# Performance work log

Hardware: AMD Instinct MI355X
Metric: run time of the kernel (lower is better)

## Reference

```python
import math
import jax, jax.numpy as jnp
import numpy as np

_EPS = 1e-8

def _nan_to_num(x):
    return jnp.where(jnp.isfinite(x), x, jnp.zeros((), x.dtype))

def _norm(x, axis=-1, keepdims=False):
    return jnp.sqrt(jnp.sum(x * x, axis=axis, keepdims=keepdims) + _EPS)

def _normalize(x, axis=-1):
    return _nan_to_num(x / _norm(x, axis=axis, keepdims=True))

def _dihedrals(X, eps=1e-7):
    # X: [B, N, A, 3]; use first 3 backbone atoms, flatten to [B, 3N, 3]
    B, N = X.shape[0], X.shape[1]
    Xf = X[:, :, :3].reshape(B, 3 * N, 3)
    dX = Xf[:, 1:] - Xf[:, :-1]
    U = _normalize(dX)
    u_2, u_1, u_0 = U[:, :-2], U[:, 1:-1], U[:, 2:]
    n_2 = _normalize(jnp.cross(u_2, u_1))
    n_1 = _normalize(jnp.cross(u_1, u_0))
    cosD = jnp.clip(jnp.sum(n_2 * n_1, -1), -1 + eps, 1 - eps)
    D = jnp.sign(jnp.sum(u_2 * n_1, -1)) * jnp.arccos(cosD)
    D = jnp.pad(D, ((0, 0), (1, 2)))
    D = D.reshape(B, N, 3)
    return jnp.concatenate([jnp.cos(D), jnp.sin(D)], axis=-1)  # [B, N, 6]

def _orientations(X):
    # X: [B, N, 3] (CA coords)
    fwd = _normalize(X[:, 1:] - X[:, :-1])
    bwd = _normalize(X[:, :-1] - X[:, 1:])
    fwd = jnp.pad(fwd, ((0, 0), (0, 1), (0, 0)))
    bwd = jnp.pad(bwd, ((0, 0), (1, 0), (0, 0)))
    return jnp.concatenate([fwd[:, :, None], bwd[:, :, None]], axis=-2)  # [B, N, 2, 3]

def _sidechains(X):
    n, origin, c = X[:, :, 0], X[:, :, 1], X[:, :, 2]
    c = _normalize(c - origin)
    n = _normalize(n - origin)
    bisector = _normalize(c + n)
    perp = _normalize(jnp.cross(c, n))
    return -bisector * math.sqrt(1.0 / 3.0) - perp * math.sqrt(2.0 / 3.0)  # [B, N, 3]

def _dist(X, coord_mask, res_idx, padding_mask, top_k, order=3):
    # X: [B, N, 3] CA coords
    B, N = X.shape[0], X.shape[1]
    cm2 = coord_mask[:, None, :] & coord_mask[:, :, None]        # [B, N, N]
    rm = ~padding_mask
    rm2 = rm[:, None, :] & rm[:, :, None]
    dX = X[:, None, :, :] - X[:, :, None, :]                     # [B, N, N, 3]
    D = cm2 * _norm(dX)                                          # masked pairwise dists
    cov = (jnp.abs(res_idx[..., None] - res_idx[..., None, :]) <= order).astype(D.dtype)
    D_cov = D * (1.0 - cov)
    seq = jnp.arange(N)
    Dseq = jnp.abs(seq[None, :] - seq[:, None]).astype(D.dtype)[None]  # [1, N, N]
    D_adjust = _nan_to_num(D_cov) + (~cm2) * (1e8 + Dseq * 1e6) + (~rm2) * 1e10
    k = min(int(top_k), N)
    # smallest-k via top_k on negated distances
    _, E_idx = jax.lax.top_k(-D_adjust, k)                       # [B, N, k]
    D_neighbors = jnp.take_along_axis(D, E_idx, axis=-1)
    coord_mask_neighbors = D_neighbors < 5e7
    residue_mask_neighbors = D_neighbors < 5e9
    return D_neighbors, E_idx, coord_mask_neighbors, residue_mask_neighbors


def setup_inputs() -> dict:
    key = jax.random.key(0)
    k1, k2 = jax.random.split(key)
    B, N = 8, 2048
    coords = jax.random.normal(k1, (B, N, 3, 3), dtype=jnp.float32) * 10.0
    coord_mask = jax.random.bernoulli(k2, 0.9, (B, N))
    res_idx = jnp.broadcast_to(jnp.arange(N, dtype=jnp.int32), (B, N))
    padding_mask = jnp.zeros((B, N), dtype=bool)
    return {"coords": coords, "coord_mask": coord_mask, "res_idx": res_idx,
            "padding_mask": padding_mask, "top_k": 30}


def reference(coords, coord_mask, res_idx, padding_mask, top_k):
    node_scalar = jnp.concatenate(
        [_dihedrals(coords), coord_mask.astype(jnp.float32)[..., None]], axis=-1)  # [B, N, 7]
    X_ca = coords[:, :, 1]
    orient = _orientations(X_ca)            # [B, N, 2, 3]
    side = _sidechains(coords)              # [B, N, 3]
    node_vector = jnp.concatenate([orient, side[:, :, None]], axis=-2)  # [B, N, 3, 3]
    D_neighbors, E_idx, cm_nb, rm_nb = _dist(X_ca, coord_mask, res_idx, padding_mask, top_k)
    return node_scalar, node_vector, D_neighbors, E_idx, cm_nb, rm_nb
```

## Files before the change

### kernel.cpp

```cpp
#include <hip/hip_runtime.h>

#define BB 8
#define NN 2048
#define KK 30
#define UNKV  0xFFFFFFFEu
#define EMPV  0xFFFFFFFFu
#define SENTJ 0xFFFFFFFFu
typedef unsigned long long ull;

__device__ __forceinline__ float norm3_eps_exact(float dx, float dy, float dz) {
    float s = __fadd_rn(__fadd_rn(__fmul_rn(dx, dx), __fmul_rn(dy, dy)), __fmul_rn(dz, dz));
    return __fsqrt_rn(__fadd_rn(s, 1e-8f));
}

__device__ __forceinline__ void normalize3f(float x, float y, float z, float* o) {
    float s = x * x + y * y + z * z + 1e-8f;
    float inv = __builtin_amdgcn_rsqf(s);
    o[0] = x * inv; o[1] = y * inv; o[2] = z * inv;
}

template <int CTRL>
__device__ __forceinline__ unsigned dppmin(unsigned v) {
    unsigned t = (unsigned)__builtin_amdgcn_update_dpp((int)v, (int)v, CTRL, 0xF, 0xF, false);
    return (t < v) ? t : v;
}
__device__ __forceinline__ unsigned wave_min_last(unsigned v) {
    v = dppmin<0xB1>(v);
    v = dppmin<0x4E>(v);
    v = dppmin<0x141>(v);
    v = dppmin<0x140>(v);
    v = dppmin<0x142>(v);
    v = dppmin<0x143>(v);
    return v;
}

__device__ __forceinline__ unsigned key_bits(const float4* __restrict__ Pb, int i, unsigned j,
                                             float xi, float yi, float zi, bool cmi_on) {
    int dd = i - (int)j;
    unsigned dj = (dd < 0) ? (unsigned)(-dd) : (unsigned)dd;
    float penB = __fadd_rn(1e8f, __fmul_rn((float)dj, 1e6f));
    float adj;
    if (cmi_on) {
        float4 p = Pb[j];
        bool cmj = ((int)__float_as_uint(p.w)) < 0;
        float nrm = norm3_eps_exact(p.x - xi, p.y - yi, p.z - zi);
        adj = cmj ? ((dj <= 3u) ? 0.0f : nrm) : penB;
    } else {
        adj = penB;
    }
    return __float_as_uint(adj);
}

__global__ __launch_bounds__(64) void prep_kernel(const float* __restrict__ coords,
                                                  const int* __restrict__ cmask,
                                                  float* __restrict__ out_scalar,
                                                  float* __restrict__ out_vec,
                                                  float4* __restrict__ P) {
    __shared__ float sm[66 * 9];
    int b  = blockIdx.x >> 5;
    int n0 = (blockIdx.x & 31) << 6;
    int tid = threadIdx.x;
    const float* gbase = coords + (size_t)b * NN * 9;
    int lof = (n0 - 1) * 9;
    for (int idx = tid; idx < 66 * 9; idx += 64) {
        int gidx = lof + idx;
        sm[idx] = ((unsigned)gidx < (unsigned)(NN * 9)) ? gbase[gidx] : 0.0f;
    }
    __syncthreads();

    const float* lbase = sm - lof;
    int n  = n0 + tid;
    int bn = b * NN + n;

    float cosv[3], sinv[3];
    #pragma unroll
    for (int t = 0; t < 3; ++t) {
        int m = 3 * n + t;
        if (m < 1 || m > 3 * NN - 3) { cosv[t] = 1.0f; sinv[t] = 0.0f; continue; }
        const float* p0 = lbase + (m - 1) * 3;
        const float* p1 = lbase + (m    ) * 3;
        const float* p2 = lbase + (m + 1) * 3;
        const float* p3 = lbase + (m + 2) * 3;
        float u2[3], u1[3], u0[3];
        normalize3f(p1[0]-p0[0], p1[1]-p0[1], p1[2]-p0[2], u2);
        normalize3f(p2[0]-p1[0], p2[1]-p1[1], p2[2]-p1[2], u1);
        normalize3f(p3[0]-p2[0], p3[1]-p2[1], p3[2]-p2[2], u0);
        float c21[3] = { u2[1]*u1[2]-u2[2]*u1[1], u2[2]*u1[0]-u2[0]*u1[2], u2[0]*u1[1]-u2[1]*u1[0] };
        float c10[3] = { u1[1]*u0[2]-u1[2]*u0[1], u1[2]*u0[0]-u1[0]*u0[2], u1[0]*u0[1]-u1[1]*u0[0] };
        float n2[3], n1v[3];
        normalize3f(c21[0], c21[1], c21[2], n2);
        normalize3f(c10[0], c10[1], c10[2], n1v);
        float cd = n2[0]*n1v[0] + n2[1]*n1v[1] + n2[2]*n1v[2];
        cd = fminf(fmaxf(cd, -1.0f + 1e-7f), 1.0f - 1e-7f);
        float sg = u2[0]*n1v[0] + u2[1]*n1v[1] + u2[2]*n1v[2];
        float sgn = (sg > 0.0f) ? 1.0f : ((sg < 0.0f) ? -1.0f : 0.0f);
        cosv[t] = (sgn == 0.0f) ? 1.0f : cd;
        sinv[t] = sgn * sqrtf(fmaxf(0.0f, 1.0f - cd * cd));
    }
    int cm = cmask[bn];
    float* os = out_scalar + (size_t)bn * 7;
    os[0] = cosv[0]; os[1] = cosv[1]; os[2] = cosv[2];
    os[3] = sinv[0]; os[4] = sinv[1]; os[5] = sinv[2];
    os[6] = cm ? 1.0f : 0.0f;

    const float* ca = lbase + (n * 3 + 1) * 3;
    float cx = ca[0], cy = ca[1], cz = ca[2];
    P[(size_t)b * NN + n] = make_float4(cx, cy, cz, __uint_as_float(cm ? 0x80000000u : 0u));

    float fwd[3] = {0.f, 0.f, 0.f}, bwd[3] = {0.f, 0.f, 0.f};
    if (n < NN - 1) {
        const float* cn = lbase + ((n + 1) * 3 + 1) * 3;
        normalize3f(cn[0]-cx, cn[1]-cy, cn[2]-cz, fwd);
    }
    if (n > 0) {
        const float* cp = lbase + ((n - 1) * 3 + 1) * 3;
        normalize3f(cp[0]-cx, cp[1]-cy, cp[2]-cz, bwd);
    }
    const float* pn = lbase + (n * 3 + 0) * 3;
    const float* pc = lbase + (n * 3 + 2) * 3;
    float cv[3], nv[3];
    normalize3f(pc[0]-cx, pc[1]-cy, pc[2]-cz, cv);
    normalize3f(pn[0]-cx, pn[1]-cy, pn[2]-cz, nv);
    float bis[3];
    normalize3f(cv[0]+nv[0], cv[1]+nv[1], cv[2]+nv[2], bis);
    float cr[3] = { cv[1]*nv[2]-cv[2]*nv[1], cv[2]*nv[0]-cv[0]*nv[2], cv[0]*nv[1]-cv[1]*nv[0] };
    float perp[3];
    normalize3f(cr[0], cr[1], cr[2], perp);
    const float s13 = 0.57735026918962576f;
    const float s23 = 0.81649658092772603f;
    float* ov = out_vec + (size_t)bn * 9;
    ov[0] = fwd[0]; ov[1] = fwd[1]; ov[2] = fwd[2];
    ov[3] = bwd[0]; ov[4] = bwd[1]; ov[5] = bwd[2];
    ov[6] = -bis[0]*s13 - perp[0]*s23;
    ov[7] = -bis[1]*s13 - perp[1]*s23;
    ov[8] = -bis[2]*s13 - perp[2]*s23;
}

__global__ __launch_bounds__(256, 8) void knn_kernel(
        const float4* __restrict__ P,
        const int* __restrict__ cmask,
        float* __restrict__ outD, float* __restrict__ outE,
        float* __restrict__ outC, float* __restrict__ outR) {
    unsigned lane = threadIdx.x & 63u;
    int wv  = threadIdx.x >> 6;
    int row = __builtin_amdgcn_readfirstlane(blockIdx.x * 4 + wv);
    int b = row >> 11, i = row & (NN - 1);

    const float4* Pb = P + (size_t)b * NN;
    bool cmi = (__builtin_amdgcn_readfirstlane(cmask[row]) != 0);

    float4 pi = Pb[i];
    float xi = pi.x, yi = pi.y, zi = pi.z;

    unsigned v1[4], j1[4], v2[4], j2[4];
    #pragma unroll
    for (int g = 0; g < 4; ++g) { v1[g] = EMPV; j1[g] = SENTJ; v2[g] = EMPV; j2[g] = SENTJ; }

    #pragma unroll
    for (int g = 0; g < 4; ++g) {
        #pragma unroll
        for (int t = 0; t < 8; ++t) {
            unsigned j = lane + 64u * (unsigned)(8 * g + t);
            unsigned kb = key_bits(Pb, i, j, xi, yi, zi, cmi);
            bool lt1 = kb < v1[g], lt2 = kb < v2[g];
            v2[g] = lt1 ? v1[g] : (lt2 ? kb : v2[g]);
            j2[g] = lt1 ? j1[g] : (lt2 ? j  : j2[g]);
            v1[g] = lt1 ? kb : v1[g];
            j1[g] = lt1 ? j  : j1[g];
        }
    }

    unsigned consumed = 0, winj = 0, lval, lj;
    {
        unsigned va = v1[0], ja = j1[0];
        if (v1[1] < va) { va = v1[1]; ja = j1[1]; }
        unsigned vb = v1[2], jb = j1[2];
        if (v1[3] < vb) { vb = v1[3]; jb = j1[3]; }
        lval = va; lj = ja;
        if (vb < va) { lval = vb; lj = jb; }
    }

    #pragma unroll 1
    for (int r = 0; r < KK; ++r) {
        unsigned mv  = wave_min_last(lval);
        unsigned s_v = (unsigned)__builtin_amdgcn_readlane((int)mv, 63);
        bool tie = (lval == s_v);
        ull bal = __ballot(tie);
        unsigned s_j;
        if (__popcll(bal) == 1) {
            int L = (int)__builtin_ctzll(bal);
            s_j = (unsigned)__builtin_amdgcn_readlane((int)lj, L);
        } else {
            unsigned cj = tie ? lj : SENTJ;
            unsigned mj = wave_min_last(cj);
            s_j = (unsigned)__builtin_amdgcn_readlane((int)mj, 63);
        }

        winj = (lane == (unsigned)r) ? s_j : winj;

        #pragma unroll
        for (int g = 0; g < 4; ++g) {
            bool match = (j1[g] == s_j);
            v1[g] = match ? v2[g] : v1[g];
            j1[g] = match ? j2[g] : j1[g];
            v2[g] = match ? UNKV : v2[g];
        }
        unsigned slot = s_j >> 6;
        bool own = (lane == (s_j & 63u));
        consumed = own ? (consumed | (1u << slot)) : consumed;

        bool need = (v1[0] == UNKV) | (v1[1] == UNKV) | (v1[2] == UNKV) | (v1[3] == UNKV);
        if (__any(need)) {
            #pragma unroll
            for (int g = 0; g < 4; ++g) {
                if (v1[g] == UNKV) {
                    unsigned nv1 = EMPV, nj1 = SENTJ, nv2 = EMPV, nj2 = SENTJ;
                    #pragma unroll 1
                    for (int t = 0; t < 8; ++t) {
                        unsigned jj = lane + 64u * (unsigned)(8 * g + t);
                        unsigned kb = ((consumed >> (unsigned)(8 * g + t)) & 1u)
                                        ? EMPV : key_bits(Pb, i, jj, xi, yi, zi, cmi);
                        bool lt1 = kb < nv1, lt2 = kb < nv2;
                        nv2 = lt1 ? nv1 : (lt2 ? kb : nv2);
                        nj2 = lt1 ? nj1 : (lt2 ? jj : nj2);
                        nv1 = lt1 ? kb : nv1;
                        nj1 = lt1 ? jj : nj1;
                    }
                    v1[g] = nv1; j1[g] = nj1; v2[g] = nv2; j2[g] = nj2;
                }
            }
        }
        unsigned va = v1[0], ja = j1[0];
        if (v1[1] < va) { va = v1[1]; ja = j1[1]; }
        unsigned vb = v1[2], jb = j1[2];
        if (v1[3] < vb) { vb = v1[3]; jb = j1[3]; }
        lval = va; lj = ja;
        if (vb < va) { lval = vb; lj = jb; }
    }

    if (lane < KK) {
        unsigned j = winj;
        float4 p = Pb[j];
        bool cmj = ((int)__float_as_uint(p.w)) < 0;
        float nrm = norm3_eps_exact(p.x - xi, p.y - yi, p.z - zi);
        float D = (cmi && cmj) ? nrm : 0.0f;
        int o = row * KK + (int)lane;
        outD[o] = D;
        outE[o] = (float)j;
        outC[o] = (D < 5.0e7f) ? 1.0f : 0.0f;
        outR[o] = (D < 5.0e9f) ? 1.0f : 0.0f;
    }
}

extern "C" void kernel_launch(void* const* d_in, const int* in_sizes, int n_in,
                              void* d_out, int out_size, void* d_ws, size_t ws_size,
                              hipStream_t stream) {
    const float* coords = (const float*)d_in[0];
    const int*   cmask  = (const int*)d_in[1];

    float* out = (float*)d_out;
    float* out_scalar = out;
    float* out_vec    = out_scalar + (size_t)BB * NN * 7;
    float* outD       = out_vec    + (size_t)BB * NN * 9;
    float* outE       = outD       + (size_t)BB * NN * KK;
    float* outC       = outE       + (size_t)BB * NN * KK;
    float* outR       = outC       + (size_t)BB * NN * KK;

    float4* P = (float4*)d_ws;

    hipLaunchKernelGGL(prep_kernel, dim3(BB * 32), dim3(64), 0, stream,
                       coords, cmask, out_scalar, out_vec, P);
    hipLaunchKernelGGL(knn_kernel, dim3(BB * NN / 4), dim3(256), 0, stream,
                       P, cmask, outD, outE, outC, outR);
}
```

Baseline: 149.6 us.

## Resolve masked rows and covalent neighbours analytically in kNN selection

Rows whose own coord mask is off now produce their neighbour list directly by sequence distance, skipping the full distance scan. For valid rows, covalent neighbours (|i-j|<=3 with valid mask) are emitted up front and excluded from the selection, which shortens the wave-level top-k loop by up to seven rounds. The launch-bounds occupancy hint is also relaxed. This relies on the tie ordering of the analytic path matching the reference selection order.

```diff
diff --git a/kernel.cpp b/kernel.cpp
--- a/kernel.cpp
+++ b/kernel.cpp
@@ -34,21 +34,16 @@
     return v;
 }
 
-__device__ __forceinline__ unsigned key_bits(const float4* __restrict__ Pb, int i, unsigned j,
-                                             float xi, float yi, float zi, bool cmi_on) {
+__device__ __forceinline__ unsigned key_on(const float4* __restrict__ Pb, int i, unsigned j,
+                                           float xi, float yi, float zi) {
     int dd = i - (int)j;
     unsigned dj = (dd < 0) ? (unsigned)(-dd) : (unsigned)dd;
+    float4 p = Pb[j];
+    bool cmj = ((int)__float_as_uint(p.w)) < 0;
+    float nrm  = norm3_eps_exact(p.x - xi, p.y - yi, p.z - zi);
     float penB = __fadd_rn(1e8f, __fmul_rn((float)dj, 1e6f));
-    float adj;
-    if (cmi_on) {
-        float4 p = Pb[j];
-        bool cmj = ((int)__float_as_uint(p.w)) < 0;
-        float nrm = norm3_eps_exact(p.x - xi, p.y - yi, p.z - zi);
-        adj = cmj ? ((dj <= 3u) ? 0.0f : nrm) : penB;
-    } else {
-        adj = penB;
-    }
-    return __float_as_uint(adj);
+    return cmj ? ((dj <= 3u) ? EMPV : __float_as_uint(nrm))
+               : __float_as_uint(penB);
 }
 
 __global__ __launch_bounds__(64) void prep_kernel(const float* __restrict__ coords,
@@ -136,7 +131,7 @@
     ov[8] = -bis[2]*s13 - perp[2]*s23;
 }
 
-__global__ __launch_bounds__(256, 8) void knn_kernel(
+__global__ __launch_bounds__(256) void knn_kernel(
         const float4* __restrict__ P,
         const int* __restrict__ cmask,
         float* __restrict__ outD, float* __restrict__ outE,
@@ -152,25 +147,55 @@
     float4 pi = Pb[i];
     float xi = pi.x, yi = pi.y, zi = pi.z;
 
+    if (!cmi) {
+        unsigned winrec = 0; int cnt = 0;
+        for (int d = 0; cnt < KK; ++d) {
+            int jm = i - d;
+            if (jm >= 0) { if (cnt == (int)lane) winrec = (unsigned)jm; ++cnt; }
+            if (d > 0 && cnt < KK) {
+                int jp = i + d;
+                if (jp < NN) { if (cnt == (int)lane) winrec = (unsigned)jp; ++cnt; }
+            }
+        }
+        if (lane < KK) {
+            int o = row * KK + (int)lane;
+            outD[o] = 0.0f;
+            outE[o] = (float)winrec;
+            outC[o] = 1.0f;
+            outR[o] = 1.0f;
+        }
+        return;
+    }
+
+    unsigned winrec = 0; int w = 0;
+    #pragma unroll
+    for (int d = -3; d <= 3; ++d) {
+        int j = i + d;
+        if (j >= 0 && j < NN) {
+            bool q = (((int)__float_as_uint(Pb[j].w)) < 0);
+            if (q) { if (w == (int)lane) winrec = (unsigned)j; ++w; }
+        }
+    }
+    int w0 = __builtin_amdgcn_readfirstlane(w);
+
     unsigned v1[4], j1[4], v2[4], j2[4];
     #pragma unroll
-    for (int g = 0; g < 4; ++g) { v1[g] = EMPV; j1[g] = SENTJ; v2[g] = EMPV; j2[g] = SENTJ; }
-
-    #pragma unroll
     for (int g = 0; g < 4; ++g) {
+        unsigned nv1 = EMPV, nj1 = SENTJ, nv2 = EMPV, nj2 = SENTJ;
         #pragma unroll
         for (int t = 0; t < 8; ++t) {
             unsigned j = lane + 64u * (unsigned)(8 * g + t);
-            unsigned kb = key_bits(Pb, i, j, xi, yi, zi, cmi);
-            bool lt1 = kb < v1[g], lt2 = kb < v2[g];
-            v2[g] = lt1 ? v1[g] : (lt2 ? kb : v2[g]);
-            j2[g] = lt1 ? j1[g] : (lt2 ? j  : j2[g]);
-            v1[g] = lt1 ? kb : v1[g];
-            j1[g] = lt1 ? j  : j1[g];
-        }
-    }
-
-    unsigned consumed = 0, winj = 0, lval, lj;
+            unsigned kb = key_on(Pb, i, j, xi, yi, zi);
+            bool lt1 = kb < nv1, lt2 = kb < nv2;
+            nv2 = lt1 ? nv1 : (lt2 ? kb : nv2);
+            nj2 = lt1 ? nj1 : (lt2 ? j  : nj2);
+            nv1 = lt1 ? kb : nv1;
+            nj1 = lt1 ? j  : nj1;
+        }
+        v1[g] = nv1; j1[g] = nj1; v2[g] = nv2; j2[g] = nj2;
+    }
+
+    unsigned consumed = 0, lval, lj;
     {
         unsigned va = v1[0], ja = j1[0];
         if (v1[1] < va) { va = v1[1]; ja = j1[1]; }
@@ -180,8 +205,7 @@
         if (vb < va) { lval = vb; lj = jb; }
     }
 
-    #pragma unroll 1
-    for (int r = 0; r < KK; ++r) {
+    for (int r = w0; r < KK; ++r) {
         unsigned mv  = wave_min_last(lval);
         unsigned s_v = (unsigned)__builtin_amdgcn_readlane((int)mv, 63);
         bool tie = (lval == s_v);
@@ -196,7 +220,7 @@
             s_j = (unsigned)__builtin_amdgcn_readlane((int)mj, 63);
         }
 
-        winj = (lane == (unsigned)r) ? s_j : winj;
+        winrec = (lane == (unsigned)r) ? s_j : winrec;
 
         #pragma unroll
         for (int g = 0; g < 4; ++g) {
@@ -219,7 +243,7 @@
                     for (int t = 0; t < 8; ++t) {
                         unsigned jj = lane + 64u * (unsigned)(8 * g + t);
                         unsigned kb = ((consumed >> (unsigned)(8 * g + t)) & 1u)
-                                        ? EMPV : key_bits(Pb, i, jj, xi, yi, zi, cmi);
+                                        ? EMPV : key_on(Pb, i, jj, xi, yi, zi);
                         bool lt1 = kb < nv1, lt2 = kb < nv2;
                         nv2 = lt1 ? nv1 : (lt2 ? kb : nv2);
                         nj2 = lt1 ? nj1 : (lt2 ? jj : nj2);
@@ -239,11 +263,11 @@
     }
 
     if (lane < KK) {
-        unsigned j = winj;
+        unsigned j = winrec;
         float4 p = Pb[j];
         bool cmj = ((int)__float_as_uint(p.w)) < 0;
         float nrm = norm3_eps_exact(p.x - xi, p.y - yi, p.z - zi);
-        float D = (cmi && cmj) ? nrm : 0.0f;
+        float D = cmj ? nrm : 0.0f;
         int o = row * KK + (int)lane;
         outD[o] = D;
         outE[o] = (float)j;
```

Result: faster. 142.8 us (-4.6%).
